# Performance work log

Measured on AMD Instinct MI355X. Metric: run time of the kernel, lower is better.

Reference implementation:

```python
import jax, jax.numpy as jnp
import numpy as np


def _ln(x, g, eps=1e-5):
    # channel LayerNorm over dim 1, unbiased=False variance
    mean = jnp.mean(x, axis=1, keepdims=True)
    var = jnp.mean((x - mean) ** 2, axis=1, keepdims=True)
    return (x - mean) * jax.lax.rsqrt(var + eps) * g


def _c11(x, w, b):
    # 1x1 conv: w (O,C), b (O,)
    return jnp.einsum('bchw,oc->bohw', x, w) + b[None, :, None, None]


def _dw(x, w, b):
    # depthwise 3x3 conv, SAME padding; w (C,1,3,3), b (C,)
    C = x.shape[1]
    y = jax.lax.conv_general_dilated(x, w, (1, 1), 'SAME',
                                     feature_group_count=C,
                                     dimension_numbers=('NCHW', 'OIHW', 'NCHW'))
    return y + b[None, :, None, None]


def _forward(F_i, F_w, g1, g2, qw1, qb1, kw1, kb1, vw1, vb1,
             qw2, qb2, kw2, kb2, vw2, vb2,
             qdw1, qdb1, kdw1, kdb1, vdw1, vdb1,
             qdw2, qdb2, kdw2, kdb2, vdw2, vdb2, lw, lb):
    B, C1, H, W = F_i.shape
    C2 = F_w.shape[1]
    HW = H * W
    fi = _ln(F_i, g1)
    fw = _ln(F_w, g2)
    # qkv = 1x1 conv -> depthwise conv; then RAW C-order reshape (torch .view)
    Qi = _dw(_c11(fi, qw1, qb1), qdw1, qdb1).reshape(B, HW, C1)
    Ki = _dw(_c11(fi, kw1, kb1), kdw1, kdb1).reshape(B, HW, C1)
    Vi = _dw(_c11(fi, vw1, vb1), vdw1, vdb1).reshape(B, C1, HW)
    Qw = _dw(_c11(fw, qw2, qb2), qdw2, qdb2).reshape(B, HW, C2)
    Kw = _dw(_c11(fw, kw2, kb2), kdw2, kdb2).reshape(B, HW, C2)
    Vw = _dw(_c11(fw, vw2, vb2), vdw2, vdb2).reshape(B, C2, HW)
    # channel cross-attention: (B,C1,HW)@(B,HW,C2) -> (B,C1,C2)
    a1 = jax.nn.softmax(jnp.einsum('bnc,bnd->bcd', Qi, Kw), axis=-1)
    a2 = jax.nn.softmax(jnp.einsum('bnc,bnd->bcd', Qw, Ki), axis=-1)
    Aw = jnp.einsum('bcd,bdn->bcn', a1, Vw).reshape(B, H, W, C2).transpose(0, 3, 1, 2)
    Ai = jnp.einsum('bcd,bdn->bcn', a2, Vi).reshape(B, H, W, C1).transpose(0, 3, 1, 2)
    cat = jnp.concatenate([Aw, Ai], axis=1)  # (B, C2+C1, H, W)
    Ct = cat.shape[1]
    flat = cat.reshape(B, Ct, HW).transpose(0, 2, 1).reshape(-1, Ct)  # (B*HW, Ct)
    out = flat @ lw.T + lb  # (B*HW, Cout)
    Cout = lb.shape[0]
    # faithful replication of torch's view/permute/view tail
    out = out.reshape(B, Cout, H, W).transpose(0, 2, 3, 1).reshape(B, Cout, H, W)
    return out + F_i + F_w


def setup_inputs() -> dict:
    key = jax.random.key(0)
    ks = jax.random.split(key, 20)
    B, C, H, W = 8, 128, 128, 128
    d = {}
    d['F_i'] = jax.random.normal(ks[0], (B, C, H, W), jnp.float32)
    d['F_w'] = jax.random.normal(ks[1], (B, C, H, W), jnp.float32)
    d['g1'] = jnp.ones((1, C, 1, 1), jnp.float32)
    d['g2'] = jnp.ones((1, C, 1, 1), jnp.float32)
    s = 1.0 / np.sqrt(C)
    i = 2
    for n in ['qw1', 'kw1', 'vw1', 'qw2', 'kw2', 'vw2']:
        d[n] = jax.random.normal(ks[i], (C, C), jnp.float32) * s
        i += 1
    for n in ['qb1', 'kb1', 'vb1', 'qb2', 'kb2', 'vb2']:
        d[n] = jnp.zeros((C,), jnp.float32)
    sd = 1.0 / 3.0
    for n in ['qdw1', 'kdw1', 'vdw1', 'qdw2', 'kdw2', 'vdw2']:
        d[n] = jax.random.normal(ks[i], (C, 1, 3, 3), jnp.float32) * sd
        i += 1
    for n in ['qdb1', 'kdb1', 'vdb1', 'qdb2', 'kdb2', 'vdb2']:
        d[n] = jnp.zeros((C,), jnp.float32)
    d['lw'] = jax.random.normal(ks[i], (C, 2 * C), jnp.float32) * (1.0 / np.sqrt(2 * C))
    d['lb'] = jnp.zeros((C,), jnp.float32)
    return d


def reference(F_i, F_w, g1, g2, qw1, qb1, kw1, kb1, vw1, vb1,
              qw2, qb2, kw2, kb2, vw2, vb2,
              qdw1, qdb1, kdw1, kdb1, vdw1, vdb1,
              qdw2, qdb2, kdw2, kdb2, vdw2, vdb2, lw, lb):
    return _forward(F_i, F_w, g1, g2, qw1, qb1, kw1, kb1, vw1, vb1,
                    qw2, qb2, kw2, kb2, vw2, vb2,
                    qdw1, qdb1, kdw1, kdb1, vdw1, vdb1,
                    qdw2, qdb2, kdw2, kdb2, vdw2, vdb2, lw, lb)
```

## Files before the change

### kernel.cpp

```cpp
#include <hip/hip_runtime.h>
#include <cstddef>
#include <cstring>

#define HW 16384
#define CC 128
#define NB 8
#define GB 4

typedef short bf16x8_t __attribute__((ext_vector_type(8)));
typedef float floatx4 __attribute__((ext_vector_type(4)));

__device__ inline unsigned short f2bf(float f) {
  unsigned u; __builtin_memcpy(&u, &f, 4);
  u += 0x7fffu + ((u >> 16) & 1u);
  return (unsigned short)(u >> 16);
}
__device__ inline float bf2f(unsigned short s) {
  unsigned u = ((unsigned)s) << 16; float f; __builtin_memcpy(&f, &u, 4);
  return f;
}

__global__ __launch_bounds__(256) void k_prep_w(
    const float* __restrict__ qw1, const float* __restrict__ kw1,
    const float* __restrict__ vw1, const float* __restrict__ qw2,
    const float* __restrict__ kw2, const float* __restrict__ vw2,
    const float* __restrict__ g1, const float* __restrict__ g2,
    const float* __restrict__ lw,
    unsigned short* __restrict__ Wsplit, unsigned short* __restrict__ lwbf) {
  const int t = threadIdx.x;
  const int m = blockIdx.y;
  if (m < 6) {
    const float* W = (m == 0) ? qw1 : (m == 1) ? kw1 : (m == 2) ? vw1
                   : (m == 3) ? qw2 : (m == 4) ? kw2 : vw2;
    const float* g = (m < 3) ? g1 : g2;
    const int idx = blockIdx.x * 256 + t;
    const int o = idx >> 4;
    const int c0 = (idx & 15) * 8;
    unsigned short* hi = Wsplit + m * 32768 + o * 128 + c0;
    unsigned short* lo = hi + 16384;
#pragma unroll
    for (int j = 0; j < 8; ++j) {
      float v = W[o * 128 + c0 + j] * g[c0 + j];
      unsigned short h = f2bf(v);
      hi[j] = h;
      lo[j] = f2bf(v - bf2f(h));
    }
  } else {
    const int idx = blockIdx.x * 256 + t;
#pragma unroll
    for (int j = 0; j < 16; ++j)
      lwbf[idx * 16 + j] = f2bf(lw[idx * 16 + j]);
  }
}

__global__ __launch_bounds__(256) void k_ln_stats(const float* __restrict__ x,
                                                  float* __restrict__ mean,
                                                  float* __restrict__ rstd) {
  int idx = blockIdx.x * 256 + threadIdx.x;
  int b = idx >> 14;
  int p = idx & (HW - 1);
  const float* xp = x + ((size_t)b << 21) + p;
  float s = 0.f, ss = 0.f;
  for (int c = 0; c < CC; ++c) {
    float v = xp[(size_t)c << 14];
    s += v;
    ss += v * v;
  }
  float m = s * (1.0f / CC);
  float var = ss * (1.0f / CC) - m * m;
  mean[idx] = m;
  rstd[idx] = rsqrtf(var + 1e-5f);
}

__global__ __launch_bounds__(256) void k_conv1x1_mfma(
    const float* __restrict__ X,
    const unsigned short* __restrict__ Whi, const unsigned short* __restrict__ Wlo,
    const float* __restrict__ bias,
    const float* __restrict__ mean, const float* __restrict__ rstd,
    float* __restrict__ Y, int b0) {
  __shared__ __align__(16) float raw[32][132];
  __shared__ __align__(16) short Bh[128][40];
  __shared__ __align__(16) short Bl[128][40];
  const int bl = blockIdx.y;
  const int b = b0 + bl;
  const int p0 = blockIdx.x * 128;
  const int t = threadIdx.x;
  const int lane = t & 63, wv = t >> 6;
  const int quad = lane >> 4, l15 = lane & 15;
  const int wr = wv >> 1, wc = wv & 1;

  const int s1c = t >> 3, s1p = (t & 7) * 16;
  const int s2p = t & 127, s2o = t >> 7;
  const float mu = mean[b * HW + p0 + s2p];
  const float rs = rstd[b * HW + p0 + s2p];

  const float* Xb = X + ((size_t)b << 21);
  floatx4 acc[4][4];
#pragma unroll
  for (int i = 0; i < 4; ++i)
#pragma unroll
    for (int j = 0; j < 4; ++j) acc[i][j] = (floatx4){0.f, 0.f, 0.f, 0.f};

  for (int k0 = 0; k0 < 128; k0 += 32) {
    {
      const float* xp = Xb + ((size_t)(k0 + s1c) << 14) + p0 + s1p;
#pragma unroll
      for (int u = 0; u < 4; ++u)
        *reinterpret_cast<float4*>(&raw[s1c][s1p + 4 * u]) =
            *reinterpret_cast<const float4*>(xp + 4 * u);
    }
    __syncthreads();
#pragma unroll
    for (int item = 0; item < 2; ++item) {
      const int oct = s2o + 2 * item;
      short th[8], tl[8];
#pragma unroll
      for (int jj = 0; jj < 8; ++jj) {
        float v = (raw[oct * 8 + jj][s2p] - mu) * rs;
        unsigned short h = f2bf(v);
        th[jj] = (short)h;
        tl[jj] = (short)f2bf(v - bf2f(h));
      }
      *reinterpret_cast<bf16x8_t*>(&Bh[s2p][oct * 8]) =
          *reinterpret_cast<bf16x8_t*>(&th[0]);
      *reinterpret_cast<bf16x8_t*>(&Bl[s2p][oct * 8]) =
          *reinterpret_cast<bf16x8_t*>(&tl[0]);
    }
    __syncthreads();
    bf16x8_t afh[4], afl[4], bfh[4], bfl[4];
#pragma unroll
    for (int i = 0; i < 4; ++i) {
      const int m = wr * 64 + i * 16 + l15;
      afh[i] = *reinterpret_cast<const bf16x8_t*>(Whi + m * 128 + k0 + quad * 8);
      afl[i] = *reinterpret_cast<const bf16x8_t*>(Wlo + m * 128 + k0 + quad * 8);
    }
#pragma unroll
    for (int j = 0; j < 4; ++j) {
      const int p = wc * 64 + j * 16 + l15;
      bfh[j] = *reinterpret_cast<const bf16x8_t*>(&Bh[p][quad * 8]);
      bfl[j] = *reinterpret_cast<const bf16x8_t*>(&Bl[p][quad * 8]);
    }
#pragma unroll
    for (int i = 0; i < 4; ++i)
#pragma unroll
      for (int j = 0; j < 4; ++j) {
        acc[i][j] = __builtin_amdgcn_mfma_f32_16x16x32_bf16(afh[i], bfh[j], acc[i][j], 0, 0, 0);
        acc[i][j] = __builtin_amdgcn_mfma_f32_16x16x32_bf16(afh[i], bfl[j], acc[i][j], 0, 0, 0);
        acc[i][j] = __builtin_amdgcn_mfma_f32_16x16x32_bf16(afl[i], bfh[j], acc[i][j], 0, 0, 0);
      }
    __syncthreads();
  }
  float* Yb = Y + ((size_t)bl << 21);
#pragma unroll
  for (int i = 0; i < 4; ++i) {
#pragma unroll
    for (int j = 0; j < 4; ++j) {
#pragma unroll
      for (int r = 0; r < 4; ++r) {
        const int o = wr * 64 + i * 16 + quad * 4 + r;
        const int p = p0 + wc * 64 + j * 16 + l15;
        Yb[((size_t)o << 14) + p] = acc[i][j][r] + bias[o];
      }
    }
  }
}

__global__ __launch_bounds__(256) void k_score_mfma(
    const float* __restrict__ Yq, const float* __restrict__ Yk,
    const float* __restrict__ qdw, const float* __restrict__ qdb,
    const float* __restrict__ kdw, const float* __restrict__ kdb,
    float* __restrict__ P) {
  __shared__ __align__(16) float raw[32][132];
  __shared__ __align__(16) short Ah[128][40];
  __shared__ __align__(16) short Al[128][40];
  __shared__ __align__(16) short Bh[128][40];
  __shared__ __align__(16) short Bl[128][40];
  const int ch = blockIdx.x;
  const int bl = blockIdx.y;
  const int t = threadIdx.x;
  const int lane = t & 63, wv = t >> 6;
  const int quad = lane >> 4, l15 = lane & 15;
  const int wr = wv >> 1, wc = wv & 1;
  const int h_loc = t >> 3;
  const int w0 = (t & 7) * 16;
  const int s2w = t & 127, s2o = t >> 7;
  const int cc = ch;
  const float* Yqb = Yq + ((size_t)bl << 21) + ((size_t)cc << 14);
  const float* Ykb = Yk + ((size_t)bl << 21) + ((size_t)cc << 14);
  const float* qwt = qdw + cc * 9;
  const float* kwt = kdw + cc * 9;
  const float qbv = qdb[cc], kbv = kdb[cc];

  floatx4 acc[4][4];
#pragma unroll
  for (int i = 0; i < 4; ++i)
#pragma unroll
    for (int j = 0; j < 4; ++j) acc[i][j] = (floatx4){0.f, 0.f, 0.f, 0.f};

  for (int k0 = 0; k0 < 128; k0 += 32) {
    const int h = k0 + h_loc;
#pragma unroll
    for (int side = 0; side < 2; ++side) {
      const float* Yc = side ? Ykb : Yqb;
      const float* wt = side ? kwt : qwt;
      const float bias = side ? kbv : qbv;
      float a[16];
#pragma unroll
      for (int j = 0; j < 16; ++j) a[j] = bias;
#pragma unroll
      for (int dy = 0; dy < 3; ++dy) {
        const int hh = h + dy - 1;
        if (hh < 0 || hh > 127) continue;
        const float* rp = Yc + (hh << 7) + w0;
        float4 f0 = *reinterpret_cast<const float4*>(rp);
        float4 f1 = *reinterpret_cast<const float4*>(rp + 4);
        float4 f2 = *reinterpret_cast<const float4*>(rp + 8);
        float4 f3 = *reinterpret_cast<const float4*>(rp + 12);
        float s[18];
        s[1] = f0.x;  s[2] = f0.y;  s[3] = f0.z;  s[4] = f0.w;
        s[5] = f1.x;  s[6] = f1.y;  s[7] = f1.z;  s[8] = f1.w;
        s[9] = f2.x;  s[10] = f2.y; s[11] = f2.z; s[12] = f2.w;
        s[13] = f3.x; s[14] = f3.y; s[15] = f3.z; s[16] = f3.w;
        s[0] = (w0 > 0) ? rp[-1] : 0.f;
        s[17] = (w0 < 112) ? rp[16] : 0.f;
        const float wa = wt[dy * 3 + 0], wb = wt[dy * 3 + 1], wc2 = wt[dy * 3 + 2];
#pragma unroll
        for (int j = 0; j < 16; ++j)
          a[j] = fmaf(s[j], wa, fmaf(s[j + 1], wb, fmaf(s[j + 2], wc2, a[j])));
      }
#pragma unroll
      for (int u = 0; u < 4; ++u)
        *reinterpret_cast<float4*>(&raw[h_loc][w0 + 4 * u]) =
            (float4){a[4 * u], a[4 * u + 1], a[4 * u + 2], a[4 * u + 3]};
      __syncthreads();
      short* dh = side ? &Bh[0][0] : &Ah[0][0];
      short* dl = side ? &Bl[0][0] : &Al[0][0];
#pragma unroll
      for (int item = 0; item < 2; ++item) {
        const int oct = s2o + 2 * item;
        short th[8], tl[8];
#pragma unroll
        for (int jj = 0; jj < 8; ++jj) {
          float v = raw[oct * 8 + jj][s2w];
          unsigned short hb = f2bf(v);
          th[jj] = (short)hb;
          tl[jj] = (short)f2bf(v - bf2f(hb));
        }
        *reinterpret_cast<bf16x8_t*>(&dh[s2w * 40 + oct * 8]) =
            *reinterpret_cast<bf16x8_t*>(&th[0]);
        *reinterpret_cast<bf16x8_t*>(&dl[s2w * 40 + oct * 8]) =
            *reinterpret_cast<bf16x8_t*>(&tl[0]);
      }
      __syncthreads();
    }
    bf16x8_t afh[4], afl[4], bfh[4], bfl[4];
#pragma unroll
    for (int i = 0; i < 4; ++i) {
      const int m = wr * 64 + i * 16 + l15;
      afh[i] = *reinterpret_cast<const bf16x8_t*>(&Ah[m][quad * 8]);
      afl[i] = *reinterpret_cast<const bf16x8_t*>(&Al[m][quad * 8]);
    }
#pragma unroll
    for (int j = 0; j < 4; ++j) {
      const int n = wc * 64 + j * 16 + l15;
      bfh[j] = *reinterpret_cast<const bf16x8_t*>(&Bh[n][quad * 8]);
      bfl[j] = *reinterpret_cast<const bf16x8_t*>(&Bl[n][quad * 8]);
    }
#pragma unroll
    for (int i = 0; i < 4; ++i)
#pragma unroll
      for (int j = 0; j < 4; ++j) {
        acc[i][j] = __builtin_amdgcn_mfma_f32_16x16x32_bf16(afh[i], bfh[j], acc[i][j], 0, 0, 0);
        acc[i][j] = __builtin_amdgcn_mfma_f32_16x16x32_bf16(afh[i], bfl[j], acc[i][j], 0, 0, 0);
        acc[i][j] = __builtin_amdgcn_mfma_f32_16x16x32_bf16(afl[i], bfh[j], acc[i][j], 0, 0, 0);
      }
  }
  float* Pp = P + ((size_t)(ch * GB + bl) << 14);
#pragma unroll
  for (int i = 0; i < 4; ++i) {
#pragma unroll
    for (int j = 0; j < 4; ++j) {
#pragma unroll
      for (int r = 0; r < 4; ++r) {
        const int c = wr * 64 + i * 16 + quad * 4 + r;
        const int d = wc * 64 + j * 16 + l15;
        Pp[c * 128 + d] = acc[i][j][r];
      }
    }
  }
}

__global__ __launch_bounds__(128) void k_reduce_softmax(
    const float* __restrict__ P, unsigned short* __restrict__ Sbf) {
  __shared__ float red[128];
  const int row = blockIdx.x;
  const int bl = row >> 7, c = row & 127;
  const int t = threadIdx.x;
  const size_t rem = ((size_t)c << 7) + t;
  float v = 0.f;
  for (int ch = 0; ch < 128; ++ch)
    v += P[((size_t)(ch * GB + bl) << 14) + rem];
  red[t] = v;
  __syncthreads();
  for (int s = 64; s > 0; s >>= 1) {
    if (t < s) red[t] = fmaxf(red[t], red[t + s]);
    __syncthreads();
  }
  float mx = red[0];
  __syncthreads();
  float e = expf(v - mx);
  red[t] = e;
  __syncthreads();
  for (int s = 64; s > 0; s >>= 1) {
    if (t < s) red[t] += red[t + s];
    __syncthreads();
  }
  Sbf[((size_t)bl << 14) + rem] = f2bf(e / red[0]);
}

__global__ __launch_bounds__(256) void k_dw_t(const float* __restrict__ Y,
                                              const float* __restrict__ Kw,
                                              const float* __restrict__ db,
                                              unsigned short* __restrict__ Vt) {
  __shared__ unsigned short T[128][33];
  const int h = blockIdx.x;
  const int c0 = blockIdx.y * 32;
  const int bl = blockIdx.z;
  const int t = threadIdx.x;
  const int cl = t >> 3;
  const int w0 = (t & 7) * 16;
  const int c = c0 + cl;
  const float* Yc = Y + ((size_t)bl << 21) + ((size_t)c << 14);
  const float* wt = Kw + c * 9;
  float a[16];
#pragma unroll
  for (int j = 0; j < 16; ++j) a[j] = db[c];
#pragma unroll
  for (int dy = 0; dy < 3; ++dy) {
    const int hh = h + dy - 1;
    if (hh < 0 || hh > 127) continue;
    const float* rp = Yc + (hh << 7) + w0;
    float4 f0 = *reinterpret_cast<const float4*>(rp);
    float4 f1 = *reinterpret_cast<const float4*>(rp + 4);
    float4 f2 = *reinterpret_cast<const float4*>(rp + 8);
    float4 f3 = *reinterpret_cast<const float4*>(rp + 12);
    float s[18];
    s[1] = f0.x;  s[2] = f0.y;  s[3] = f0.z;  s[4] = f0.w;
    s[5] = f1.x;  s[6] = f1.y;  s[7] = f1.z;  s[8] = f1.w;
    s[9] = f2.x;  s[10] = f2.y; s[11] = f2.z; s[12] = f2.w;
    s[13] = f3.x; s[14] = f3.y; s[15] = f3.z; s[16] = f3.w;
    s[0] = (w0 > 0) ? rp[-1] : 0.f;
    s[17] = (w0 < 112) ? rp[16] : 0.f;
    const float wa = wt[dy * 3 + 0], wb = wt[dy * 3 + 1], wc2 = wt[dy * 3 + 2];
#pragma unroll
    for (int j = 0; j < 16; ++j)
      a[j] = fmaf(s[j], wa, fmaf(s[j + 1], wb, fmaf(s[j + 2], wc2, a[j])));
  }
#pragma unroll
  for (int j = 0; j < 16; ++j) T[w0 + j][cl] = f2bf(a[j]);
  __syncthreads();
  const int w = t >> 1, half = t & 1;
  unsigned short tmp[16];
#pragma unroll
  for (int j = 0; j < 16; ++j) tmp[j] = T[w][half * 16 + j];
  uint4 v0, v1;
  unsigned* vp0 = reinterpret_cast<unsigned*>(&v0);
  unsigned* vp1 = reinterpret_cast<unsigned*>(&v1);
#pragma unroll
  for (int j = 0; j < 4; ++j) {
    vp0[j] = (unsigned)tmp[2 * j] | ((unsigned)tmp[2 * j + 1] << 16);
    vp1[j] = (unsigned)tmp[8 + 2 * j] | ((unsigned)tmp[8 + 2 * j + 1] << 16);
  }
  unsigned short* dst = Vt + ((size_t)bl << 21) + ((size_t)((h << 7) + w) << 7)
                        + c0 + half * 16;
  *reinterpret_cast<uint4*>(dst) = v0;
  *reinterpret_cast<uint4*>(dst + 8) = v1;
}

__global__ __launch_bounds__(256) void k_av_mfma(
    const unsigned short* __restrict__ Sbf, const unsigned short* __restrict__ Vt,
    unsigned short* __restrict__ O) {
  const int bl = blockIdx.y;
  const int p0 = blockIdx.x * 128;
  const int t = threadIdx.x;
  const int lane = t & 63, wv = t >> 6;
  const int quad = lane >> 4, l15 = lane & 15;
  const int wr = wv >> 1, wc = wv & 1;
  const unsigned short* Sb = Sbf + ((size_t)bl << 14);
  floatx4 acc[4][4];
#pragma unroll
  for (int i = 0; i < 4; ++i)
#pragma unroll
    for (int j = 0; j < 4; ++j) acc[i][j] = (floatx4){0.f, 0.f, 0.f, 0.f};
  const unsigned short* Vb = Vt + ((size_t)bl << 21);
#pragma unroll
  for (int d0 = 0; d0 < 128; d0 += 32) {
    bf16x8_t af[4], bf[4];
#pragma unroll
    for (int i = 0; i < 4; ++i) {
      const int m = wr * 64 + i * 16 + l15;
      af[i] = *reinterpret_cast<const bf16x8_t*>(Sb + m * 128 + d0 + quad * 8);
    }
#pragma unroll
    for (int j = 0; j < 4; ++j) {
      const int p = p0 + wc * 64 + j * 16 + l15;
      bf[j] = *reinterpret_cast<const bf16x8_t*>(Vb + ((size_t)p << 7) + d0 + quad * 8);
    }
#pragma unroll
    for (int i = 0; i < 4; ++i)
#pragma unroll
      for (int j = 0; j < 4; ++j)
        acc[i][j] = __builtin_amdgcn_mfma_f32_16x16x32_bf16(af[i], bf[j], acc[i][j], 0, 0, 0);
  }
  unsigned short* Ob = O + ((size_t)bl << 21);
#pragma unroll
  for (int i = 0; i < 4; ++i) {
#pragma unroll
    for (int j = 0; j < 4; ++j) {
#pragma unroll
      for (int r = 0; r < 4; ++r) {
        const int c = wr * 64 + i * 16 + quad * 4 + r;
        const int p = p0 + wc * 64 + j * 16 + l15;
        Ob[((size_t)c << 14) + p] = f2bf(acc[i][j][r]);
      }
    }
  }
}

__global__ __launch_bounds__(256) void k_final2_mfma(
    const unsigned short* __restrict__ A1, const unsigned short* __restrict__ A2,
    const unsigned short* __restrict__ lwbf, const float* __restrict__ lb,
    const float* __restrict__ Fi, const float* __restrict__ Fw,
    float* __restrict__ out, int b0) {
  const int c2 = blockIdx.x;
  const int bl = blockIdx.y;
  const int b = b0 + bl;
  const int t = threadIdx.x;
  const int lane = t & 63, wv = t >> 6;
  const int quad = lane >> 4, l15 = lane & 15;
  const int wr = wv >> 1, wc = wv & 1;
  floatx4 acc[4][4];
#pragma unroll
  for (int i = 0; i < 4; ++i)
#pragma unroll
    for (int j = 0; j < 4; ++j) acc[i][j] = (floatx4){0.f, 0.f, 0.f, 0.f};
#pragma unroll
  for (int phase = 0; phase < 2; ++phase) {
    const unsigned short* Ub = (phase ? A2 : A1) + ((size_t)bl << 21) + c2 * 128;
#pragma unroll
    for (int d0 = 0; d0 < 128; d0 += 32) {
      bf16x8_t af[4], bf[4];
#pragma unroll
      for (int i = 0; i < 4; ++i) {
        const int m = wr * 64 + i * 16 + l15;
        af[i] = *reinterpret_cast<const bf16x8_t*>(
            lwbf + m * 256 + phase * 128 + d0 + quad * 8);
      }
#pragma unroll
      for (int j = 0; j < 4; ++j) {
        const int n = wc * 64 + j * 16 + l15;
        bf[j] = *reinterpret_cast<const bf16x8_t*>(Ub + ((size_t)n << 14) + d0 + quad * 8);
      }
#pragma unroll
      for (int i = 0; i < 4; ++i)
#pragma unroll
        for (int j = 0; j < 4; ++j)
          acc[i][j] = __builtin_amdgcn_mfma_f32_16x16x32_bf16(af[i], bf[j], acc[i][j], 0, 0, 0);
    }
  }
  const size_t obase = ((size_t)b << 21) + ((size_t)c2 << 14);
#pragma unroll
  for (int i = 0; i < 4; ++i) {
#pragma unroll
    for (int j = 0; j < 4; ++j) {
#pragma unroll
      for (int r = 0; r < 4; ++r) {
        const int h2 = wr * 64 + i * 16 + quad * 4 + r;
        const int w2 = wc * 64 + j * 16 + l15;
        const size_t a = obase + ((size_t)h2 << 7) + w2;
        out[a] = acc[i][j][r] + lb[h2] + Fi[a] + Fw[a];
      }
    }
  }
}

extern "C" void kernel_launch(void* const* d_in, const int* in_sizes, int n_in,
                              void* d_out, int out_size, void* d_ws, size_t ws_size,
                              hipStream_t stream) {
  const float* F_i  = (const float*)d_in[0];
  const float* F_w  = (const float*)d_in[1];
  const float* g1   = (const float*)d_in[2];
  const float* g2   = (const float*)d_in[3];
  const float* qw1  = (const float*)d_in[4];
  const float* kw1  = (const float*)d_in[5];
  const float* vw1  = (const float*)d_in[6];
  const float* qw2  = (const float*)d_in[7];
  const float* kw2  = (const float*)d_in[8];
  const float* vw2  = (const float*)d_in[9];
  const float* qb1  = (const float*)d_in[10];
  const float* kb1  = (const float*)d_in[11];
  const float* vb1  = (const float*)d_in[12];
  const float* qb2  = (const float*)d_in[13];
  const float* kb2  = (const float*)d_in[14];
  const float* vb2  = (const float*)d_in[15];
  const float* qdw1 = (const float*)d_in[16];
  const float* kdw1 = (const float*)d_in[17];
  const float* vdw1 = (const float*)d_in[18];
  const float* qdw2 = (const float*)d_in[19];
  const float* kdw2 = (const float*)d_in[20];
  const float* vdw2 = (const float*)d_in[21];
  const float* qdb1 = (const float*)d_in[22];
  const float* kdb1 = (const float*)d_in[23];
  const float* vdb1 = (const float*)d_in[24];
  const float* qdb2 = (const float*)d_in[25];
  const float* kdb2 = (const float*)d_in[26];
  const float* vdb2 = (const float*)d_in[27];
  const float* lw   = (const float*)d_in[28];
  const float* lb   = (const float*)d_in[29];
  float* out = (float*)d_out;

  char* w = (char*)d_ws;
  const size_t NTOT = (size_t)NB * HW;
  float* meanI = (float*)w; w += NTOT * 4;
  float* rstdI = (float*)w; w += NTOT * 4;
  float* meanW = (float*)w; w += NTOT * 4;
  float* rstdW = (float*)w; w += NTOT * 4;
  unsigned short* Sbf = (unsigned short*)w; w += (size_t)GB * HW * 2;
  unsigned short* Wsplit = (unsigned short*)w; w += 6 * 32768 * 2;
  unsigned short* lwbf = (unsigned short*)w; w += 32768 * 2;
  float* P     = (float*)w; w += (size_t)128 * GB * HW * 4;
  float* Yq    = (float*)w; w += ((size_t)GB << 21) * 4;
  char*  Ykreg = w;         w += ((size_t)GB << 21) * 4;
  float* Yk    = (float*)Ykreg;
  unsigned short* Vt = (unsigned short*)Ykreg;
  unsigned short* A2 = (unsigned short*)(Ykreg + ((size_t)GB << 21) * 2);
  unsigned short* A1 = (unsigned short*)w; w += ((size_t)GB << 21) * 2;

  const unsigned short* Wh0 = Wsplit + 0 * 32768;
  const unsigned short* Wh1 = Wsplit + 1 * 32768;
  const unsigned short* Wh2 = Wsplit + 2 * 32768;
  const unsigned short* Wh3 = Wsplit + 3 * 32768;
  const unsigned short* Wh4 = Wsplit + 4 * 32768;
  const unsigned short* Wh5 = Wsplit + 5 * 32768;

  dim3 blk(256);
  k_prep_w<<<dim3(8, 7), blk, 0, stream>>>(qw1, kw1, vw1, qw2, kw2, vw2,
                                           g1, g2, lw, Wsplit, lwbf);
  k_ln_stats<<<dim3(512), blk, 0, stream>>>(F_i, meanI, rstdI);
  k_ln_stats<<<dim3(512), blk, 0, stream>>>(F_w, meanW, rstdW);

  for (int b0 = 0; b0 < NB; b0 += GB) {
    k_conv1x1_mfma<<<dim3(128, GB), blk, 0, stream>>>(F_i, Wh0, Wh0 + 16384, qb1, meanI, rstdI, Yq, b0);
    k_conv1x1_mfma<<<dim3(128, GB), blk, 0, stream>>>(F_w, Wh4, Wh4 + 16384, kb2, meanW, rstdW, Yk, b0);
    k_score_mfma<<<dim3(128, GB), blk, 0, stream>>>(Yq, Yk, qdw1, qdb1, kdw2, kdb2, P);
    k_reduce_softmax<<<dim3(GB * 128), dim3(128), 0, stream>>>(P, Sbf);
    k_conv1x1_mfma<<<dim3(128, GB), blk, 0, stream>>>(F_w, Wh5, Wh5 + 16384, vb2, meanW, rstdW, Yq, b0);
    k_dw_t<<<dim3(128, 4, GB), blk, 0, stream>>>(Yq, vdw2, vdb2, Vt);
    k_av_mfma<<<dim3(128, GB), blk, 0, stream>>>(Sbf, Vt, A1);

    k_conv1x1_mfma<<<dim3(128, GB), blk, 0, stream>>>(F_w, Wh3, Wh3 + 16384, qb2, meanW, rstdW, Yq, b0);
    k_conv1x1_mfma<<<dim3(128, GB), blk, 0, stream>>>(F_i, Wh1, Wh1 + 16384, kb1, meanI, rstdI, Yk, b0);
    k_score_mfma<<<dim3(128, GB), blk, 0, stream>>>(Yq, Yk, qdw2, qdb2, kdw1, kdb1, P);
    k_reduce_softmax<<<dim3(GB * 128), dim3(128), 0, stream>>>(P, Sbf);
    k_conv1x1_mfma<<<dim3(128, GB), blk, 0, stream>>>(F_i, Wh2, Wh2 + 16384, vb1, meanI, rstdI, Yq, b0);
    k_dw_t<<<dim3(128, 4, GB), blk, 0, stream>>>(Yq, vdw1, vdb1, Vt);
    k_av_mfma<<<dim3(128, GB), blk, 0, stream>>>(Sbf, Vt, A2);

    k_final2_mfma<<<dim3(128, GB), blk, 0, stream>>>(A1, A2, lwbf, lb, F_i, F_w, out, b0);
  }
}
```

Before: 808.5 us.

## Drop LDS staging in 1x1 conv, load inputs directly into MFMA fragments

The 1x1 conv kernel no longer stages input tiles through shared memory. Each lane now loads its 8 channel values straight from global memory, normalizes them and splits them into bf16 hi/lo fragments in registers, which removes the LDS traffic and all three barriers per k-step. The pixel tile is halved to 64 with twice the grid and launch bounds ask for 4 blocks per CU. LN stats also process two pixels per thread with float2 loads. In exchange, the strided per-channel global loads are only 16 contiguous floats per quad, so coalescing may suffer, and the weight fragments are reloaded by twice as many blocks.

```diff
diff --git a/kernel.cpp b/kernel.cpp
--- a/kernel.cpp
+++ b/kernel.cpp
@@ -57,108 +57,101 @@
                                                   float* __restrict__ mean,
                                                   float* __restrict__ rstd) {
   int idx = blockIdx.x * 256 + threadIdx.x;
-  int b = idx >> 14;
-  int p = idx & (HW - 1);
+  int p2 = idx * 2;
+  int b = p2 >> 14;
+  int p = p2 & (HW - 1);
   const float* xp = x + ((size_t)b << 21) + p;
-  float s = 0.f, ss = 0.f;
+  float s0 = 0.f, ss0 = 0.f, s1 = 0.f, ss1 = 0.f;
   for (int c = 0; c < CC; ++c) {
-    float v = xp[(size_t)c << 14];
-    s += v;
-    ss += v * v;
-  }
-  float m = s * (1.0f / CC);
-  float var = ss * (1.0f / CC) - m * m;
-  mean[idx] = m;
-  rstd[idx] = rsqrtf(var + 1e-5f);
-}
-
-__global__ __launch_bounds__(256) void k_conv1x1_mfma(
+    float2 v = *reinterpret_cast<const float2*>(xp + ((size_t)c << 14));
+    s0 += v.x; ss0 += v.x * v.x;
+    s1 += v.y; ss1 += v.y * v.y;
+  }
+  float m0 = s0 * (1.0f / CC), m1 = s1 * (1.0f / CC);
+  float var0 = ss0 * (1.0f / CC) - m0 * m0;
+  float var1 = ss1 * (1.0f / CC) - m1 * m1;
+  *reinterpret_cast<float2*>(mean + p2) = (float2){m0, m1};
+  *reinterpret_cast<float2*>(rstd + p2) =
+      (float2){rsqrtf(var0 + 1e-5f), rsqrtf(var1 + 1e-5f)};
+}
+
+__global__ __launch_bounds__(256, 4) void k_conv1x1_mfma(
     const float* __restrict__ X,
     const unsigned short* __restrict__ Whi, const unsigned short* __restrict__ Wlo,
     const float* __restrict__ bias,
     const float* __restrict__ mean, const float* __restrict__ rstd,
     float* __restrict__ Y, int b0) {
-  __shared__ __align__(16) float raw[32][132];
-  __shared__ __align__(16) short Bh[128][40];
-  __shared__ __align__(16) short Bl[128][40];
   const int bl = blockIdx.y;
   const int b = b0 + bl;
-  const int p0 = blockIdx.x * 128;
+  const int p0 = blockIdx.x * 64;
   const int t = threadIdx.x;
   const int lane = t & 63, wv = t >> 6;
   const int quad = lane >> 4, l15 = lane & 15;
   const int wr = wv >> 1, wc = wv & 1;
 
-  const int s1c = t >> 3, s1p = (t & 7) * 16;
-  const int s2p = t & 127, s2o = t >> 7;
-  const float mu = mean[b * HW + p0 + s2p];
-  const float rs = rstd[b * HW + p0 + s2p];
-
   const float* Xb = X + ((size_t)b << 21);
-  floatx4 acc[4][4];
+  int pj[2]; float muj[2], rsj[2];
+#pragma unroll
+  for (int j = 0; j < 2; ++j) {
+    pj[j] = p0 + wc * 32 + j * 16 + l15;
+    muj[j] = mean[b * HW + pj[j]];
+    rsj[j] = rstd[b * HW + pj[j]];
+  }
+
+  floatx4 acc[4][2];
 #pragma unroll
   for (int i = 0; i < 4; ++i)
 #pragma unroll
-    for (int j = 0; j < 4; ++j) acc[i][j] = (floatx4){0.f, 0.f, 0.f, 0.f};
+    for (int j = 0; j < 2; ++j) acc[i][j] = (floatx4){0.f, 0.f, 0.f, 0.f};
 
   for (int k0 = 0; k0 < 128; k0 += 32) {
-    {
-      const float* xp = Xb + ((size_t)(k0 + s1c) << 14) + p0 + s1p;
-#pragma unroll
-      for (int u = 0; u < 4; ++u)
-        *reinterpret_cast<float4*>(&raw[s1c][s1p + 4 * u]) =
-            *reinterpret_cast<const float4*>(xp + 4 * u);
-    }
-    __syncthreads();
-#pragma unroll
-    for (int item = 0; item < 2; ++item) {
-      const int oct = s2o + 2 * item;
-      short th[8], tl[8];
-#pragma unroll
-      for (int jj = 0; jj < 8; ++jj) {
-        float v = (raw[oct * 8 + jj][s2p] - mu) * rs;
-        unsigned short h = f2bf(v);
-        th[jj] = (short)h;
-        tl[jj] = (short)f2bf(v - bf2f(h));
-      }
-      *reinterpret_cast<bf16x8_t*>(&Bh[s2p][oct * 8]) =
-          *reinterpret_cast<bf16x8_t*>(&th[0]);
-      *reinterpret_cast<bf16x8_t*>(&Bl[s2p][oct * 8]) =
-          *reinterpret_cast<bf16x8_t*>(&tl[0]);
-    }
-    __syncthreads();
-    bf16x8_t afh[4], afl[4], bfh[4], bfl[4];
+    bf16x8_t afh[4], afl[4];
 #pragma unroll
     for (int i = 0; i < 4; ++i) {
       const int m = wr * 64 + i * 16 + l15;
       afh[i] = *reinterpret_cast<const bf16x8_t*>(Whi + m * 128 + k0 + quad * 8);
       afl[i] = *reinterpret_cast<const bf16x8_t*>(Wlo + m * 128 + k0 + quad * 8);
     }
-#pragma unroll
-    for (int j = 0; j < 4; ++j) {
-      const int p = wc * 64 + j * 16 + l15;
-      bfh[j] = *reinterpret_cast<const bf16x8_t*>(&Bh[p][quad * 8]);
-      bfl[j] = *reinterpret_cast<const bf16x8_t*>(&Bl[p][quad * 8]);
+    float xv[2][8];
+#pragma unroll
+    for (int j = 0; j < 2; ++j) {
+      const float* xp = Xb + ((size_t)(k0 + quad * 8) << 14) + pj[j];
+#pragma unroll
+      for (int jj = 0; jj < 8; ++jj)
+        xv[j][jj] = xp[(size_t)jj << 14];
+    }
+    bf16x8_t bfh[2], bfl[2];
+#pragma unroll
+    for (int j = 0; j < 2; ++j) {
+      short th[8], tl[8];
+#pragma unroll
+      for (int jj = 0; jj < 8; ++jj) {
+        float v = (xv[j][jj] - muj[j]) * rsj[j];
+        unsigned short h = f2bf(v);
+        th[jj] = (short)h;
+        tl[jj] = (short)f2bf(v - bf2f(h));
+      }
+      bfh[j] = *reinterpret_cast<bf16x8_t*>(&th[0]);
+      bfl[j] = *reinterpret_cast<bf16x8_t*>(&tl[0]);
     }
 #pragma unroll
     for (int i = 0; i < 4; ++i)
 #pragma unroll
-      for (int j = 0; j < 4; ++j) {
+      for (int j = 0; j < 2; ++j) {
         acc[i][j] = __builtin_amdgcn_mfma_f32_16x16x32_bf16(afh[i], bfh[j], acc[i][j], 0, 0, 0);
         acc[i][j] = __builtin_amdgcn_mfma_f32_16x16x32_bf16(afh[i], bfl[j], acc[i][j], 0, 0, 0);
         acc[i][j] = __builtin_amdgcn_mfma_f32_16x16x32_bf16(afl[i], bfh[j], acc[i][j], 0, 0, 0);
       }
-    __syncthreads();
   }
   float* Yb = Y + ((size_t)bl << 21);
 #pragma unroll
   for (int i = 0; i < 4; ++i) {
 #pragma unroll
-    for (int j = 0; j < 4; ++j) {
+    for (int j = 0; j < 2; ++j) {
 #pragma unroll
       for (int r = 0; r < 4; ++r) {
         const int o = wr * 64 + i * 16 + quad * 4 + r;
-        const int p = p0 + wc * 64 + j * 16 + l15;
+        const int p = p0 + wc * 32 + j * 16 + l15;
         Yb[((size_t)o << 14) + p] = acc[i][j][r] + bias[o];
       }
     }
@@ -546,23 +539,23 @@
   dim3 blk(256);
   k_prep_w<<<dim3(8, 7), blk, 0, stream>>>(qw1, kw1, vw1, qw2, kw2, vw2,
                                            g1, g2, lw, Wsplit, lwbf);
-  k_ln_stats<<<dim3(512), blk, 0, stream>>>(F_i, meanI, rstdI);
-  k_ln_stats<<<dim3(512), blk, 0, stream>>>(F_w, meanW, rstdW);
+  k_ln_stats<<<dim3(256), blk, 0, stream>>>(F_i, meanI, rstdI);
+  k_ln_stats<<<dim3(256), blk, 0, stream>>>(F_w, meanW, rstdW);
 
   for (int b0 = 0; b0 < NB; b0 += GB) {
-    k_conv1x1_mfma<<<dim3(128, GB), blk, 0, stream>>>(F_i, Wh0, Wh0 + 16384, qb1, meanI, rstdI, Yq, b0);
-    k_conv1x1_mfma<<<dim3(128, GB), blk, 0, stream>>>(F_w, Wh4, Wh4 + 16384, kb2, meanW, rstdW, Yk, b0);
+    k_conv1x1_mfma<<<dim3(256, GB), blk, 0, stream>>>(F_i, Wh0, Wh0 + 16384, qb1, meanI, rstdI, Yq, b0);
+    k_conv1x1_mfma<<<dim3(256, GB), blk, 0, stream>>>(F_w, Wh4, Wh4 + 16384, kb2, meanW, rstdW, Yk, b0);
     k_score_mfma<<<dim3(128, GB), blk, 0, stream>>>(Yq, Yk, qdw1, qdb1, kdw2, kdb2, P);
     k_reduce_softmax<<<dim3(GB * 128), dim3(128), 0, stream>>>(P, Sbf);
-    k_conv1x1_mfma<<<dim3(128, GB), blk, 0, stream>>>(F_w, Wh5, Wh5 + 16384, vb2, meanW, rstdW, Yq, b0);
+    k_conv1x1_mfma<<<dim3(256, GB), blk, 0, stream>>>(F_w, Wh5, Wh5 + 16384, vb2, meanW, rstdW, Yq, b0);
     k_dw_t<<<dim3(128, 4, GB), blk, 0, stream>>>(Yq, vdw2, vdb2, Vt);
     k_av_mfma<<<dim3(128, GB), blk, 0, stream>>>(Sbf, Vt, A1);
 
-    k_conv1x1_mfma<<<dim3(128, GB), blk, 0, stream>>>(F_w, Wh3, Wh3 + 16384, qb2, meanW, rstdW, Yq, b0);
-    k_conv1x1_mfma<<<dim3(128, GB), blk, 0, stream>>>(F_i, Wh1, Wh1 + 16384, kb1, meanI, rstdI, Yk, b0);
+    k_conv1x1_mfma<<<dim3(256, GB), blk, 0, stream>>>(F_w, Wh3, Wh3 + 16384, qb2, meanW, rstdW, Yq, b0);
+    k_conv1x1_mfma<<<dim3(256, GB), blk, 0, stream>>>(F_i, Wh1, Wh1 + 16384, kb1, meanI, rstdI, Yk, b0);
     k_score_mfma<<<dim3(128, GB), blk, 0, stream>>>(Yq, Yk, qdw2, qdb2, kdw1, kdb1, P);
     k_reduce_softmax<<<dim3(GB * 128), dim3(128), 0, stream>>>(P, Sbf);
-    k_conv1x1_mfma<<<dim3(128, GB), blk, 0, stream>>>(F_i, Wh2, Wh2 + 16384, vb1, meanI, rstdI, Yq, b0);
+    k_conv1x1_mfma<<<dim3(256, GB), blk, 0, stream>>>(F_i, Wh2, Wh2 + 16384, vb1, meanI, rstdI, Yq, b0);
     k_dw_t<<<dim3(128, 4, GB), blk, 0, stream>>>(Yq, vdw1, vdb1, Vt);
     k_av_mfma<<<dim3(128, GB), blk, 0, stream>>>(Sbf, Vt, A2);
 
```

Measured after the change: 875.1 us. +8.2%, slower.

## Split score kernel over output-row halves and vectorize LayerNorm stats loads

Applied to the files above, without the earlier changes.

The score kernel grid gains a z dimension of 2, so each block computes 64 of the 128 C1 rows of the per-chunk score tile. The Q side now builds only its 64-column slice, while the K side is still fully recomputed in each block. The aim is to double the block count from 512 and raise occupancy through smaller accumulators and shared memory. The cost is duplicated K depthwise conv and bf16 split work plus two extra barriers per k-step. Separately, k_ln_stats processes two pixels per thread with float2 loads and launches half as many blocks.

```diff
diff --git a/kernel.cpp b/kernel.cpp
--- a/kernel.cpp
+++ b/kernel.cpp
@@ -57,19 +57,22 @@
                                                   float* __restrict__ mean,
                                                   float* __restrict__ rstd) {
   int idx = blockIdx.x * 256 + threadIdx.x;
-  int b = idx >> 14;
-  int p = idx & (HW - 1);
+  int p2 = idx * 2;
+  int b = p2 >> 14;
+  int p = p2 & (HW - 1);
   const float* xp = x + ((size_t)b << 21) + p;
-  float s = 0.f, ss = 0.f;
+  float s0 = 0.f, ss0 = 0.f, s1 = 0.f, ss1 = 0.f;
   for (int c = 0; c < CC; ++c) {
-    float v = xp[(size_t)c << 14];
-    s += v;
-    ss += v * v;
-  }
-  float m = s * (1.0f / CC);
-  float var = ss * (1.0f / CC) - m * m;
-  mean[idx] = m;
-  rstd[idx] = rsqrtf(var + 1e-5f);
+    float2 v = *reinterpret_cast<const float2*>(xp + ((size_t)c << 14));
+    s0 += v.x; ss0 += v.x * v.x;
+    s1 += v.y; ss1 += v.y * v.y;
+  }
+  float m0 = s0 * (1.0f / CC), m1 = s1 * (1.0f / CC);
+  float var0 = ss0 * (1.0f / CC) - m0 * m0;
+  float var1 = ss1 * (1.0f / CC) - m1 * m1;
+  *reinterpret_cast<float2*>(mean + p2) = (float2){m0, m1};
+  *reinterpret_cast<float2*>(rstd + p2) =
+      (float2){rsqrtf(var0 + 1e-5f), rsqrtf(var1 + 1e-5f)};
 }
 
 __global__ __launch_bounds__(256) void k_conv1x1_mfma(
@@ -171,47 +174,88 @@
     const float* __restrict__ kdw, const float* __restrict__ kdb,
     float* __restrict__ P) {
   __shared__ __align__(16) float raw[32][132];
-  __shared__ __align__(16) short Ah[128][40];
-  __shared__ __align__(16) short Al[128][40];
+  __shared__ __align__(16) short Ah[64][40];
+  __shared__ __align__(16) short Al[64][40];
   __shared__ __align__(16) short Bh[128][40];
   __shared__ __align__(16) short Bl[128][40];
   const int ch = blockIdx.x;
   const int bl = blockIdx.y;
+  const int chalf = blockIdx.z;
   const int t = threadIdx.x;
   const int lane = t & 63, wv = t >> 6;
   const int quad = lane >> 4, l15 = lane & 15;
   const int wr = wv >> 1, wc = wv & 1;
   const int h_loc = t >> 3;
   const int w0 = (t & 7) * 16;
+  const int wlq = (t & 7) * 8;
+  const int w0q = wlq + chalf * 64;
   const int s2w = t & 127, s2o = t >> 7;
-  const int cc = ch;
-  const float* Yqb = Yq + ((size_t)bl << 21) + ((size_t)cc << 14);
-  const float* Ykb = Yk + ((size_t)bl << 21) + ((size_t)cc << 14);
-  const float* qwt = qdw + cc * 9;
-  const float* kwt = kdw + cc * 9;
-  const float qbv = qdb[cc], kbv = kdb[cc];
-
-  floatx4 acc[4][4];
-#pragma unroll
-  for (int i = 0; i < 4; ++i)
+  const int qtw = t & 63, qto = t >> 6;
+  const float* Yqb = Yq + ((size_t)bl << 21) + ((size_t)ch << 14);
+  const float* Ykb = Yk + ((size_t)bl << 21) + ((size_t)ch << 14);
+  const float* qwt = qdw + ch * 9;
+  const float* kwt = kdw + ch * 9;
+  const float qbv = qdb[ch], kbv = kdb[ch];
+
+  floatx4 acc[2][4];
+#pragma unroll
+  for (int i = 0; i < 2; ++i)
 #pragma unroll
     for (int j = 0; j < 4; ++j) acc[i][j] = (floatx4){0.f, 0.f, 0.f, 0.f};
 
   for (int k0 = 0; k0 < 128; k0 += 32) {
     const int h = k0 + h_loc;
-#pragma unroll
-    for (int side = 0; side < 2; ++side) {
-      const float* Yc = side ? Ykb : Yqb;
-      const float* wt = side ? kwt : qwt;
-      const float bias = side ? kbv : qbv;
-      float a[16];
-#pragma unroll
-      for (int j = 0; j < 16; ++j) a[j] = bias;
+    {
+      float a[8];
+#pragma unroll
+      for (int j = 0; j < 8; ++j) a[j] = qbv;
 #pragma unroll
       for (int dy = 0; dy < 3; ++dy) {
         const int hh = h + dy - 1;
         if (hh < 0 || hh > 127) continue;
-        const float* rp = Yc + (hh << 7) + w0;
+        const float* rp = Yqb + (hh << 7) + w0q;
+        float4 f0 = *reinterpret_cast<const float4*>(rp);
+        float4 f1 = *reinterpret_cast<const float4*>(rp + 4);
+        float s[10];
+        s[1] = f0.x; s[2] = f0.y; s[3] = f0.z; s[4] = f0.w;
+        s[5] = f1.x; s[6] = f1.y; s[7] = f1.z; s[8] = f1.w;
+        s[0] = (w0q > 0) ? rp[-1] : 0.f;
+        s[9] = (w0q < 120) ? rp[8] : 0.f;
+        const float wa = qwt[dy * 3 + 0], wb = qwt[dy * 3 + 1], wc2 = qwt[dy * 3 + 2];
+#pragma unroll
+        for (int j = 0; j < 8; ++j)
+          a[j] = fmaf(s[j], wa, fmaf(s[j + 1], wb, fmaf(s[j + 2], wc2, a[j])));
+      }
+      *reinterpret_cast<float4*>(&raw[h_loc][wlq]) =
+          (float4){a[0], a[1], a[2], a[3]};
+      *reinterpret_cast<float4*>(&raw[h_loc][wlq + 4]) =
+          (float4){a[4], a[5], a[6], a[7]};
+    }
+    __syncthreads();
+    {
+      short th[8], tl[8];
+#pragma unroll
+      for (int jj = 0; jj < 8; ++jj) {
+        float v = raw[qto * 8 + jj][qtw];
+        unsigned short hb = f2bf(v);
+        th[jj] = (short)hb;
+        tl[jj] = (short)f2bf(v - bf2f(hb));
+      }
+      *reinterpret_cast<bf16x8_t*>(&Ah[qtw][qto * 8]) =
+          *reinterpret_cast<bf16x8_t*>(&th[0]);
+      *reinterpret_cast<bf16x8_t*>(&Al[qtw][qto * 8]) =
+          *reinterpret_cast<bf16x8_t*>(&tl[0]);
+    }
+    __syncthreads();
+    {
+      float a[16];
+#pragma unroll
+      for (int j = 0; j < 16; ++j) a[j] = kbv;
+#pragma unroll
+      for (int dy = 0; dy < 3; ++dy) {
+        const int hh = h + dy - 1;
+        if (hh < 0 || hh > 127) continue;
+        const float* rp = Ykb + (hh << 7) + w0;
         float4 f0 = *reinterpret_cast<const float4*>(rp);
         float4 f1 = *reinterpret_cast<const float4*>(rp + 4);
         float4 f2 = *reinterpret_cast<const float4*>(rp + 8);
@@ -223,7 +267,7 @@
         s[13] = f3.x; s[14] = f3.y; s[15] = f3.z; s[16] = f3.w;
         s[0] = (w0 > 0) ? rp[-1] : 0.f;
         s[17] = (w0 < 112) ? rp[16] : 0.f;
-        const float wa = wt[dy * 3 + 0], wb = wt[dy * 3 + 1], wc2 = wt[dy * 3 + 2];
+        const float wa = kwt[dy * 3 + 0], wb = kwt[dy * 3 + 1], wc2 = kwt[dy * 3 + 2];
 #pragma unroll
         for (int j = 0; j < 16; ++j)
           a[j] = fmaf(s[j], wa, fmaf(s[j + 1], wb, fmaf(s[j + 2], wc2, a[j])));
@@ -232,9 +276,9 @@
       for (int u = 0; u < 4; ++u)
         *reinterpret_cast<float4*>(&raw[h_loc][w0 + 4 * u]) =
             (float4){a[4 * u], a[4 * u + 1], a[4 * u + 2], a[4 * u + 3]};
-      __syncthreads();
-      short* dh = side ? &Bh[0][0] : &Ah[0][0];
-      short* dl = side ? &Bl[0][0] : &Al[0][0];
+    }
+    __syncthreads();
+    {
 #pragma unroll
       for (int item = 0; item < 2; ++item) {
         const int oct = s2o + 2 * item;
@@ -246,17 +290,17 @@
           th[jj] = (short)hb;
           tl[jj] = (short)f2bf(v - bf2f(hb));
         }
-        *reinterpret_cast<bf16x8_t*>(&dh[s2w * 40 + oct * 8]) =
+        *reinterpret_cast<bf16x8_t*>(&Bh[s2w][oct * 8]) =
             *reinterpret_cast<bf16x8_t*>(&th[0]);
-        *reinterpret_cast<bf16x8_t*>(&dl[s2w * 40 + oct * 8]) =
+        *reinterpret_cast<bf16x8_t*>(&Bl[s2w][oct * 8]) =
             *reinterpret_cast<bf16x8_t*>(&tl[0]);
       }
-      __syncthreads();
-    }
-    bf16x8_t afh[4], afl[4], bfh[4], bfl[4];
-#pragma unroll
-    for (int i = 0; i < 4; ++i) {
-      const int m = wr * 64 + i * 16 + l15;
+    }
+    __syncthreads();
+    bf16x8_t afh[2], afl[2], bfh[4], bfl[4];
+#pragma unroll
+    for (int i = 0; i < 2; ++i) {
+      const int m = wr * 32 + i * 16 + l15;
       afh[i] = *reinterpret_cast<const bf16x8_t*>(&Ah[m][quad * 8]);
       afl[i] = *reinterpret_cast<const bf16x8_t*>(&Al[m][quad * 8]);
     }
@@ -267,7 +311,7 @@
       bfl[j] = *reinterpret_cast<const bf16x8_t*>(&Bl[n][quad * 8]);
     }
 #pragma unroll
-    for (int i = 0; i < 4; ++i)
+    for (int i = 0; i < 2; ++i)
 #pragma unroll
       for (int j = 0; j < 4; ++j) {
         acc[i][j] = __builtin_amdgcn_mfma_f32_16x16x32_bf16(afh[i], bfh[j], acc[i][j], 0, 0, 0);
@@ -277,12 +321,12 @@
   }
   float* Pp = P + ((size_t)(ch * GB + bl) << 14);
 #pragma unroll
-  for (int i = 0; i < 4; ++i) {
+  for (int i = 0; i < 2; ++i) {
 #pragma unroll
     for (int j = 0; j < 4; ++j) {
 #pragma unroll
       for (int r = 0; r < 4; ++r) {
-        const int c = wr * 64 + i * 16 + quad * 4 + r;
+        const int c = chalf * 64 + wr * 32 + i * 16 + quad * 4 + r;
         const int d = wc * 64 + j * 16 + l15;
         Pp[c * 128 + d] = acc[i][j][r];
       }
@@ -546,13 +590,13 @@
   dim3 blk(256);
   k_prep_w<<<dim3(8, 7), blk, 0, stream>>>(qw1, kw1, vw1, qw2, kw2, vw2,
                                            g1, g2, lw, Wsplit, lwbf);
-  k_ln_stats<<<dim3(512), blk, 0, stream>>>(F_i, meanI, rstdI);
-  k_ln_stats<<<dim3(512), blk, 0, stream>>>(F_w, meanW, rstdW);
+  k_ln_stats<<<dim3(256), blk, 0, stream>>>(F_i, meanI, rstdI);
+  k_ln_stats<<<dim3(256), blk, 0, stream>>>(F_w, meanW, rstdW);
 
   for (int b0 = 0; b0 < NB; b0 += GB) {
     k_conv1x1_mfma<<<dim3(128, GB), blk, 0, stream>>>(F_i, Wh0, Wh0 + 16384, qb1, meanI, rstdI, Yq, b0);
     k_conv1x1_mfma<<<dim3(128, GB), blk, 0, stream>>>(F_w, Wh4, Wh4 + 16384, kb2, meanW, rstdW, Yk, b0);
-    k_score_mfma<<<dim3(128, GB), blk, 0, stream>>>(Yq, Yk, qdw1, qdb1, kdw2, kdb2, P);
+    k_score_mfma<<<dim3(128, GB, 2), blk, 0, stream>>>(Yq, Yk, qdw1, qdb1, kdw2, kdb2, P);
     k_reduce_softmax<<<dim3(GB * 128), dim3(128), 0, stream>>>(P, Sbf);
     k_conv1x1_mfma<<<dim3(128, GB), blk, 0, stream>>>(F_w, Wh5, Wh5 + 16384, vb2, meanW, rstdW, Yq, b0);
     k_dw_t<<<dim3(128, 4, GB), blk, 0, stream>>>(Yq, vdw2, vdb2, Vt);
@@ -560,7 +604,7 @@
 
     k_conv1x1_mfma<<<dim3(128, GB), blk, 0, stream>>>(F_w, Wh3, Wh3 + 16384, qb2, meanW, rstdW, Yq, b0);
     k_conv1x1_mfma<<<dim3(128, GB), blk, 0, stream>>>(F_i, Wh1, Wh1 + 16384, kb1, meanI, rstdI, Yk, b0);
-    k_score_mfma<<<dim3(128, GB), blk, 0, stream>>>(Yq, Yk, qdw2, qdb2, kdw1, kdb1, P);
+    k_score_mfma<<<dim3(128, GB, 2), blk, 0, stream>>>(Yq, Yk, qdw2, qdb2, kdw1, kdb1, P);
     k_reduce_softmax<<<dim3(GB * 128), dim3(128), 0, stream>>>(P, Sbf);
     k_conv1x1_mfma<<<dim3(128, GB), blk, 0, stream>>>(F_i, Wh2, Wh2 + 16384, vb1, meanI, rstdI, Yq, b0);
     k_dw_t<<<dim3(128, 4, GB), blk, 0, stream>>>(Yq, vdw1, vdb1, Vt);
```

New measurement: 877.1 us. 8.5% more time.
